# Kernel tuning notes

Measured on AMD Instinct MI355X. Metric: run time of the kernel, lower is better.

## Reference

```python
import jax, jax.numpy as jnp
import numpy as np

N_NODES = 50000
N_EDGES = 640000
HID = 128
EDGE_FEAT = 4
NUM_G = 20
R_MIN, R_MAX = 0.0, 10.0

def setup_inputs() -> dict:
    key = jax.random.key(0)
    ks = jax.random.split(key, 16)
    s = lambda d: 1.0 / np.sqrt(d)
    return {
        'h': jax.random.normal(ks[0], (N_NODES, HID), jnp.float32),
        'x': jax.random.normal(ks[1], (N_NODES, 3), jnp.float32),
        'edge_index': jax.random.randint(ks[2], (2, N_EDGES), 0, N_NODES, dtype=jnp.int64),
        'mask_ligand': jnp.ones((N_NODES,), jnp.float32),
        'edge_attr': jax.random.normal(ks[3], (N_EDGES, EDGE_FEAT), jnp.float32),
        'We1': jax.random.normal(ks[4], (2*HID+EDGE_FEAT+NUM_G, HID), jnp.float32) * s(2*HID+EDGE_FEAT+NUM_G),
        'be1': jnp.zeros((HID,), jnp.float32),
        'We2': jax.random.normal(ks[5], (HID, HID), jnp.float32) * s(HID),
        'be2': jnp.zeros((HID,), jnp.float32),
        'Winf': jax.random.normal(ks[6], (HID, 1), jnp.float32) * s(HID),
        'binf': jnp.zeros((1,), jnp.float32),
        'Wx1': jax.random.normal(ks[7], (HID, HID), jnp.float32) * s(HID),
        'bx1': jnp.zeros((HID,), jnp.float32),
        'Wx2': jax.random.normal(ks[8], (HID, 1), jnp.float32) * 0.001 * s(HID),
        'Wn1': jax.random.normal(ks[9], (2*HID, HID), jnp.float32) * s(2*HID),
        'bn1': jnp.zeros((HID,), jnp.float32),
        'Wn2': jax.random.normal(ks[10], (HID, HID), jnp.float32) * s(HID),
        'bn2': jnp.zeros((HID,), jnp.float32),
    }

def reference(h, x, edge_index, mask_ligand, edge_attr,
              We1, be1, We2, be2, Winf, binf, Wx1, bx1, Wx2, Wn1, bn1, Wn2, bn2):
    n = h.shape[0]
    src, dst = edge_index[0], edge_index[1]
    hi, hj = h[dst], h[src]                      # [E, H] gathers
    rel_x = x[dst] - x[src]                      # [E, 3]
    d_sq = jnp.sum(rel_x**2, axis=-1, keepdims=True)  # [E, 1]
    d = jnp.sqrt(d_sq + 1e-8)
    # GaussianSmearing(r_min=0, r_max=10, num_gaussians=20)
    offset = jnp.linspace(R_MIN, R_MAX, NUM_G, dtype=h.dtype)
    coeff = -0.5 / (offset[1] - offset[0])**2
    d_feat = jnp.exp(coeff * (d - offset)**2)    # [E, 20]
    edge_feat = jnp.concatenate([d_feat, edge_attr], axis=-1)
    # edge MLP (2 layers, silu, act_last=True)
    z = jnp.concatenate([hi, hj, edge_feat], axis=-1)
    mij = jax.nn.silu(jax.nn.silu(z @ We1 + be1) @ We2 + be2)  # [E, H]
    eij = jax.nn.sigmoid(mij @ Winf + binf)      # [E, 1]
    mi = jax.ops.segment_sum(mij * eij, dst, num_segments=n)   # [N, H]
    # node MLP (2 layers, silu, no act on last)
    nz = jnp.concatenate([mi, h], axis=-1)
    h_out = h + (jax.nn.silu(nz @ Wn1 + bn1) @ Wn2 + bn2)
    # coordinate update
    xg = jnp.tanh(jax.nn.silu(mij @ Wx1 + bx1) @ Wx2)          # [E, 1]
    delta_x = jax.ops.segment_sum(rel_x / (d + 1.0) * xg, dst, num_segments=n)
    x_out = x + delta_x * mask_ligand[:, None]
    return h_out, x_out
```

## Files before the change

### kernel.cpp

```cpp
#include <hip/hip_runtime.h>
#include <math.h>

#define NN 50000
#define NE 640000
#define H 128
#define EPB 64
#define NPB 64
#define ZB 280
#define BB 136
#define KP1 288
#define NZB 264
#define NBPAD 50176
#define HISTB (NE / 256)
#define CONVB 464
#define ALLOCB (NBPAD / 256)
#define HCONVB 3125
#define N4OUT ((NN * H + NN * 3) / 4)
#define ZOB ((N4OUT + 255) / 256)

typedef __attribute__((ext_vector_type(8))) unsigned short u16x8;
typedef __attribute__((ext_vector_type(8))) __bf16 bf16x8;
typedef __attribute__((ext_vector_type(2))) __bf16 bf16x2;
typedef __attribute__((ext_vector_type(4))) float f32x4;

__device__ __forceinline__ float frcp(float x) {
#if __has_builtin(__builtin_amdgcn_rcpf)
    return __builtin_amdgcn_rcpf(x);
#else
    return 1.0f / x;
#endif
}

__device__ __forceinline__ float silu_f(float v) {
    return v * frcp(1.0f + __expf(-v));
}

__device__ __forceinline__ float sigmoid_f(float v) {
    return frcp(1.0f + __expf(-v));
}

__device__ __forceinline__ float tanh_f(float v) {
    return 1.0f - 2.0f * frcp(1.0f + __expf(2.0f * v));
}

__device__ __forceinline__ unsigned short f2bf(float f) {
    unsigned int u = __builtin_bit_cast(unsigned int, f);
    u += 0x7FFFu + ((u >> 16) & 1u);
    return (unsigned short)(u >> 16);
}

__device__ __forceinline__ float bf2f(unsigned short s) {
    unsigned int u = ((unsigned int)s) << 16;
    return __builtin_bit_cast(float, u);
}

__device__ __forceinline__ unsigned int pkbf(float lo, float hi) {
#if __has_builtin(__builtin_amdgcn_cvt_pk_bf16_f32)
    bf16x2 v = __builtin_amdgcn_cvt_pk_bf16_f32(lo, hi);
    unsigned int r; __builtin_memcpy(&r, &v, 4); return r;
#else
    return (unsigned int)f2bf(lo) | ((unsigned int)f2bf(hi) << 16);
#endif
}

__device__ __forceinline__ f32x4 mfma16(u16x8 a, u16x8 b, f32x4 c) {
    return __builtin_amdgcn_mfma_f32_16x16x32_bf16(
        __builtin_bit_cast(bf16x8, a), __builtin_bit_cast(bf16x8, b), c, 0, 0, 0);
}

__global__ __launch_bounds__(256) void init_small_kernel(
    float4* __restrict__ p, int n4)
{
    int i = blockIdx.x * 256 + threadIdx.x;
    if (i < n4) p[i] = make_float4(0.f, 0.f, 0.f, 0.f);
}

__global__ __launch_bounds__(256) void hist_conv_zero_kernel(
    const int* __restrict__ ei, int* __restrict__ cnt, int histBlocks,
    const float* __restrict__ We1, const float* __restrict__ We2,
    const float* __restrict__ Wx1, const float* __restrict__ Wn1,
    const float* __restrict__ Wn2,
    unsigned short* __restrict__ w1t, unsigned short* __restrict__ w2t,
    unsigned short* __restrict__ wx1t, unsigned short* __restrict__ wn1t,
    unsigned short* __restrict__ wn2t,
    float4* __restrict__ out4)
{
    int b = blockIdx.x, t = threadIdx.x;
    if (b < histBlocks) {
        atomicAdd(&cnt[ei[NE + b * 256 + t]], 1);
        return;
    }
    b -= histBlocks;
    if (b < CONVB) {
        int i = b * 256 + t;
        const int S1 = 128 * KP1;
        const int S2 = 128 * 128;
        const int S3 = 128 * 256;
        if (i < S1) {
            int n = i / KP1, k = i % KP1;
            w1t[i] = (k < 280) ? f2bf(We1[k * H + n]) : (unsigned short)0;
        } else if (i < S1 + S2) {
            int j = i - S1; int n = j / H, k = j % H;
            w2t[j] = f2bf(We2[k * H + n]);
        } else if (i < S1 + 2 * S2) {
            int j = i - S1 - S2; int n = j / H, k = j % H;
            wx1t[j] = f2bf(Wx1[k * H + n]);
        } else if (i < S1 + 2 * S2 + S3) {
            int j = i - S1 - 2 * S2; int n = j / 256, k = j % 256;
            wn1t[j] = f2bf(Wn1[k * H + n]);
        } else if (i < S1 + 3 * S2 + S3) {
            int j = i - S1 - 2 * S2 - S3; int n = j / H, k = j % H;
            wn2t[j] = f2bf(Wn2[k * H + n]);
        }
        return;
    }
    b -= CONVB;
    int i = b * 256 + t;
    if (i < N4OUT) out4[i] = make_float4(0.f, 0.f, 0.f, 0.f);
}

__global__ __launch_bounds__(256) void alloc_kernel(
    const int* __restrict__ cnt, int* __restrict__ cur, int* __restrict__ gtot)
{
    int t = threadIdx.x;
    int d = blockIdx.x * 256 + t;
    int v = cnt[d];
    int incl = v;
    #pragma unroll
    for (int o = 1; o < 64; o <<= 1) {
        int u = __shfl_up(incl, o, 64);
        if ((t & 63) >= o) incl += u;
    }
    int total = __shfl(incl, 63, 64);
    int base = 0;
    if ((t & 63) == 63) base = atomicAdd(gtot, total);
    base = __shfl(base, 63, 64);
    cur[d] = base + incl - v;
}

__global__ __launch_bounds__(256) void scatter_hconv_kernel(
    const int* __restrict__ ei, const float* __restrict__ edge_attr,
    int* __restrict__ cur, uint4* __restrict__ epay,
    const float* __restrict__ h, unsigned short* __restrict__ hb)
{
    int b = blockIdx.x, t = threadIdx.x;
    if (b < NE / 256) {
        int i = b * 256 + t;
        int s = ei[i], d = ei[NE + i];
        float4 ea = ((const float4*)edge_attr)[i];
        int p = atomicAdd(&cur[d], 1);
        uint4 pv = { (unsigned)s, (unsigned)d, pkbf(ea.x, ea.y), pkbf(ea.z, ea.w) };
        epay[p] = pv;
        return;
    }
    int j = (b - NE / 256) * 256 + t;
    const float4* hp = (const float4*)h + (size_t)j * 2;
    float4 a = hp[0], c = hp[1];
    uint4 pk = { pkbf(a.x, a.y), pkbf(a.z, a.w), pkbf(c.x, c.y), pkbf(c.z, c.w) };
    ((uint4*)hb)[j] = pk;
}

__global__ __launch_bounds__(512, 6) void edge_kernel(
    const float* __restrict__ h, const float* __restrict__ x,
    const int* __restrict__ ei, const float* __restrict__ edge_attr,
    const unsigned short* __restrict__ w1t, const float* __restrict__ be1,
    const unsigned short* __restrict__ w2t, const float* __restrict__ be2,
    const float* __restrict__ Winf, const float* __restrict__ binf,
    const unsigned short* __restrict__ wx1t, const float* __restrict__ bx1,
    const float* __restrict__ Wx2,
    const uint4* __restrict__ epay, const unsigned short* __restrict__ hb,
    float* __restrict__ mi, float* __restrict__ dx)
{
    __shared__ unsigned short zs[EPB * ZB + 8];
    __shared__ float relx_s[EPB][3];
    __shared__ float eij_acc[EPB];
    __shared__ float xg_acc[EPB];
    __shared__ int dst_s[EPB];
    __shared__ float winf_s[H];
    __shared__ float wx2_s[H];

    unsigned short* m1 = zs;
    unsigned short* m2 = zs + EPB * BB;

    const int t = threadIdx.x;
    int bid = blockIdx.x;
    if ((gridDim.x & 7) == 0) {
        int cpx = gridDim.x >> 3;
        bid = (bid & 7) * cpx + (bid >> 3);
    }
    const int e0 = bid * EPB;
    const bool srt = (epay != nullptr);

    if (t >= 128 && t < 256) {
        winf_s[t - 128] = Winf[t - 128];
        wx2_s[t - 128] = Wx2[t - 128];
    } else if (t >= 256 && t < 320) {
        eij_acc[t - 256] = binf[0];
        xg_acc[t - 256] = 0.f;
    } else if (t == 320) {
        uint4 zf = {0u, 0u, 0u, 0u};
        *(uint4*)(zs + EPB * ZB) = zf;
    }

    {
        int e = t >> 3, l = t & 7;
        unsigned short* zr = zs + e * ZB;
        if (srt) {
            uint4 pv = epay[e0 + e];
            const uint4* hd = (const uint4*)(hb + (size_t)pv.y * H);
            const uint4* hs = (const uint4*)(hb + (size_t)pv.x * H);
            uint4 a0 = hd[l * 2], a1 = hd[l * 2 + 1];
            *(uint4*)(zr + l * 16) = a0;
            *(uint4*)(zr + l * 16 + 8) = a1;
            uint4 c0 = hs[l * 2], c1 = hs[l * 2 + 1];
            *(uint4*)(zr + 128 + l * 16) = c0;
            *(uint4*)(zr + 128 + l * 16 + 8) = c1;
        } else {
            int s = ei[e0 + e], d = ei[NE + e0 + e];
            const float4* hd = (const float4*)(h + (size_t)d * H);
            const float4* hs = (const float4*)(h + (size_t)s * H);
            float4 v0 = hd[l * 4 + 0], v1 = hd[l * 4 + 1];
            float4 v2 = hd[l * 4 + 2], v3 = hd[l * 4 + 3];
            uint4 p0 = { pkbf(v0.x, v0.y), pkbf(v0.z, v0.w), pkbf(v1.x, v1.y), pkbf(v1.z, v1.w) };
            uint4 p1 = { pkbf(v2.x, v2.y), pkbf(v2.z, v2.w), pkbf(v3.x, v3.y), pkbf(v3.z, v3.w) };
            *(uint4*)(zr + l * 16) = p0;
            *(uint4*)(zr + l * 16 + 8) = p1;
            float4 w0 = hs[l * 4 + 0], w1 = hs[l * 4 + 1];
            float4 w2 = hs[l * 4 + 2], w3 = hs[l * 4 + 3];
            uint4 q0 = { pkbf(w0.x, w0.y), pkbf(w0.z, w0.w), pkbf(w1.x, w1.y), pkbf(w1.z, w1.w) };
            uint4 q1 = { pkbf(w2.x, w2.y), pkbf(w2.z, w2.w), pkbf(w3.x, w3.y), pkbf(w3.z, w3.w) };
            *(uint4*)(zr + 128 + l * 16) = q0;
            *(uint4*)(zr + 128 + l * 16 + 8) = q1;
        }
    }
    if (t < EPB) {
        unsigned short* zr = zs + t * ZB;
        int s, d;
        if (srt) {
            uint4 pv = epay[e0 + t];
            s = (int)pv.x; d = (int)pv.y;
            *(unsigned int*)(zr + 276) = pv.z;
            *(unsigned int*)(zr + 278) = pv.w;
        } else {
            s = ei[e0 + t]; d = ei[NE + e0 + t];
            #pragma unroll
            for (int j = 0; j < 4; j++)
                zr[276 + j] = f2bf(edge_attr[(size_t)(e0 + t) * 4 + j]);
        }
        dst_s[t] = d;
        float rx = x[d * 3 + 0] - x[s * 3 + 0];
        float ry = x[d * 3 + 1] - x[s * 3 + 1];
        float rz = x[d * 3 + 2] - x[s * 3 + 2];
        float d2 = rx * rx + ry * ry + rz * rz;
        float dd = sqrtf(d2 + 1e-8f);
        float inv = frcp(dd + 1.0f);
        relx_s[t][0] = rx * inv;
        relx_s[t][1] = ry * inv;
        relx_s[t][2] = rz * inv;
        const float step = 10.0f / 19.0f;
        const float coeff = -0.5f / (step * step);
        #pragma unroll
        for (int g = 0; g < 20; g++) {
            float df = dd - step * (float)g;
            zr[256 + g] = f2bf(__expf(coeff * df * df));
        }
    }
    __syncthreads();

    const int wv = t >> 6, lane = t & 63;
    const int quad = lane >> 4, r16 = lane & 15;
    const int F = wv * 16;
    const int f0 = F + quad * 4;

    {
        f32x4 acc[4] = {};
        #pragma unroll
        for (int ks = 0; ks < KP1 / 32; ks++) {
            int ko = ks * 32 + quad * 8;
            u16x8 a = *(const u16x8*)(w1t + (size_t)(F + r16) * KP1 + ko);
            #pragma unroll
            for (int ci = 0; ci < 4; ci++) {
                u16x8 b = *(const u16x8*)(zs + (ci * 16 + r16) * ZB + ko);
                acc[ci] = mfma16(a, b, acc[ci]);
            }
        }
        __syncthreads();
        float4 bv = *(const float4*)(be1 + f0);
        #pragma unroll
        for (int ci = 0; ci < 4; ci++) {
            int e = ci * 16 + r16;
            float s0 = silu_f(acc[ci][0] + bv.x);
            float s1 = silu_f(acc[ci][1] + bv.y);
            float s2 = silu_f(acc[ci][2] + bv.z);
            float s3 = silu_f(acc[ci][3] + bv.w);
            uint2 p = { pkbf(s0, s1), pkbf(s2, s3) };
            *(uint2*)(m1 + e * BB + f0) = p;
        }
    }
    __syncthreads();

    {
        f32x4 acc[4] = {};
        #pragma unroll
        for (int ks = 0; ks < H / 32; ks++) {
            int ko = ks * 32 + quad * 8;
            u16x8 a = *(const u16x8*)(w2t + (size_t)(F + r16) * H + ko);
            #pragma unroll
            for (int ci = 0; ci < 4; ci++) {
                u16x8 b = *(const u16x8*)(m1 + (ci * 16 + r16) * BB + ko);
                acc[ci] = mfma16(a, b, acc[ci]);
            }
        }
        float4 bv = *(const float4*)(be2 + f0);
        float4 wf = *(const float4*)(winf_s + f0);
        float ep[4];
        #pragma unroll
        for (int ci = 0; ci < 4; ci++) {
            int e = ci * 16 + r16;
            float s0 = silu_f(acc[ci][0] + bv.x);
            float s1 = silu_f(acc[ci][1] + bv.y);
            float s2 = silu_f(acc[ci][2] + bv.z);
            float s3 = silu_f(acc[ci][3] + bv.w);
            ep[ci] = s0 * wf.x + s1 * wf.y + s2 * wf.z + s3 * wf.w;
            uint2 p = { pkbf(s0, s1), pkbf(s2, s3) };
            *(uint2*)(m2 + e * BB + f0) = p;
        }
        #pragma unroll
        for (int ci = 0; ci < 4; ci++) {
            ep[ci] += __shfl_xor(ep[ci], 16, 64);
            ep[ci] += __shfl_xor(ep[ci], 32, 64);
        }
        if (quad == 0) {
            #pragma unroll
            for (int ci = 0; ci < 4; ci++)
                atomicAdd(&eij_acc[ci * 16 + r16], ep[ci]);
        }
    }
    __syncthreads();

    if (t < EPB) eij_acc[t] = sigmoid_f(eij_acc[t]);

    {
        f32x4 acc[4] = {};
        #pragma unroll
        for (int ks = 0; ks < H / 32; ks++) {
            int ko = ks * 32 + quad * 8;
            u16x8 a = *(const u16x8*)(wx1t + (size_t)(F + r16) * H + ko);
            #pragma unroll
            for (int ci = 0; ci < 4; ci++) {
                u16x8 b = *(const u16x8*)(m2 + (ci * 16 + r16) * BB + ko);
                acc[ci] = mfma16(a, b, acc[ci]);
            }
        }
        float4 bv = *(const float4*)(bx1 + f0);
        float4 wf = *(const float4*)(wx2_s + f0);
        float xp[4];
        #pragma unroll
        for (int ci = 0; ci < 4; ci++) {
            xp[ci] = silu_f(acc[ci][0] + bv.x) * wf.x
                   + silu_f(acc[ci][1] + bv.y) * wf.y
                   + silu_f(acc[ci][2] + bv.z) * wf.z
                   + silu_f(acc[ci][3] + bv.w) * wf.w;
        }
        #pragma unroll
        for (int ci = 0; ci < 4; ci++) {
            xp[ci] += __shfl_xor(xp[ci], 16, 64);
            xp[ci] += __shfl_xor(xp[ci], 32, 64);
        }
        if (quad == 0) {
            #pragma unroll
            for (int ci = 0; ci < 4; ci++)
                atomicAdd(&xg_acc[ci * 16 + r16], xp[ci]);
        }
    }
    __syncthreads();

    if (t < 128) {
        const int k = t;
        float acc = 0.f;
        int rs = 0;
        #pragma unroll
        for (int c = 0; c < EPB; c += 8) {
            float v[8];
            #pragma unroll
            for (int j = 0; j < 8; j++)
                v[j] = bf2f(m2[(c + j) * BB + k]) * eij_acc[c + j];
            #pragma unroll
            for (int j = 0; j < 8; j++) {
                int e = c + j;
                acc += v[j];
                if (e == EPB - 1 || dst_s[e + 1] != dst_s[e]) {
                    float* p = &mi[(size_t)dst_s[e] * H + k];
                    if (srt && rs > 0 && e < EPB - 1) *p = acc;
                    else atomicAdd(p, acc);
                    acc = 0.f;
                    rs = e + 1;
                }
            }
        }
    } else if (t < 131) {
        const int dd = t - 128;
        float acc = 0.f;
        int rs = 0;
        #pragma unroll
        for (int c = 0; c < EPB; c += 8) {
            float v[8];
            #pragma unroll
            for (int j = 0; j < 8; j++)
                v[j] = relx_s[c + j][dd] * tanh_f(xg_acc[c + j]);
            #pragma unroll
            for (int j = 0; j < 8; j++) {
                int e = c + j;
                acc += v[j];
                if (e == EPB - 1 || dst_s[e + 1] != dst_s[e]) {
                    float* p = &dx[(size_t)dst_s[e] * 3 + dd];
                    if (srt && rs > 0 && e < EPB - 1) *p = acc;
                    else atomicAdd(p, acc);
                    acc = 0.f;
                    rs = e + 1;
                }
            }
        }
    }
}

__global__ __launch_bounds__(512, 6) void node_kernel(
    const float* __restrict__ h, const float* __restrict__ x,
    const float* __restrict__ mask,
    const unsigned short* __restrict__ wn1t, const float* __restrict__ bn1,
    const unsigned short* __restrict__ wn2t, const float* __restrict__ bn2,
    const unsigned short* __restrict__ hb,
    float* __restrict__ mi_hout, float* __restrict__ dx_xout)
{
    __shared__ unsigned short nzs[NPB * NZB];

    unsigned short* nbuf = nzs;

    const int t = threadIdx.x;
    const int n0 = blockIdx.x * NPB;

    {
        int r = t >> 3, l = t & 7;
        int n = n0 + r;
        unsigned short* zr = nzs + r * NZB;
        if (n < NN) {
            const float4* mi4 = (const float4*)(mi_hout + (size_t)n * H);
            float4 v0 = mi4[l * 4 + 0], v1 = mi4[l * 4 + 1];
            float4 v2 = mi4[l * 4 + 2], v3 = mi4[l * 4 + 3];
            uint4 p0 = { pkbf(v0.x, v0.y), pkbf(v0.z, v0.w), pkbf(v1.x, v1.y), pkbf(v1.z, v1.w) };
            uint4 p1 = { pkbf(v2.x, v2.y), pkbf(v2.z, v2.w), pkbf(v3.x, v3.y), pkbf(v3.z, v3.w) };
            *(uint4*)(zr + l * 16) = p0;
            *(uint4*)(zr + l * 16 + 8) = p1;
            if (hb) {
                const uint4* hs = (const uint4*)(hb + (size_t)n * H);
                *(uint4*)(zr + 128 + l * 16) = hs[l * 2];
                *(uint4*)(zr + 128 + l * 16 + 8) = hs[l * 2 + 1];
            } else {
                const float4* h4 = (const float4*)(h + (size_t)n * H);
                float4 w0 = h4[l * 4 + 0], w1 = h4[l * 4 + 1];
                float4 w2 = h4[l * 4 + 2], w3 = h4[l * 4 + 3];
                uint4 q0 = { pkbf(w0.x, w0.y), pkbf(w0.z, w0.w), pkbf(w1.x, w1.y), pkbf(w1.z, w1.w) };
                uint4 q1 = { pkbf(w2.x, w2.y), pkbf(w2.z, w2.w), pkbf(w3.x, w3.y), pkbf(w3.z, w3.w) };
                *(uint4*)(zr + 128 + l * 16) = q0;
                *(uint4*)(zr + 128 + l * 16 + 8) = q1;
            }
        } else {
            uint4 zf = {0u, 0u, 0u, 0u};
            *(uint4*)(zr + l * 16) = zf;
            *(uint4*)(zr + l * 16 + 8) = zf;
            *(uint4*)(zr + 128 + l * 16) = zf;
            *(uint4*)(zr + 128 + l * 16 + 8) = zf;
        }
    }

    float xo = 0.f;
    int xn = -1, xdim = 0;
    if (t < NPB * 3) {
        int r = t / 3; xdim = t % 3;
        int n = n0 + r;
        if (n < NN) {
            xn = n;
            xo = x[(size_t)n * 3 + xdim] + dx_xout[(size_t)n * 3 + xdim] * mask[n];
        }
    }
    __syncthreads();

    if (xn >= 0) dx_xout[(size_t)xn * 3 + xdim] = xo;

    const int wv = t >> 6, lane = t & 63;
    const int quad = lane >> 4, r16 = lane & 15;
    const int F = wv * 16;
    const int f0 = F + quad * 4;

    {
        f32x4 acc[4] = {};
        #pragma unroll
        for (int ks = 0; ks < 2 * H / 32; ks++) {
            int ko = ks * 32 + quad * 8;
            u16x8 a = *(const u16x8*)(wn1t + (size_t)(F + r16) * (2 * H) + ko);
            #pragma unroll
            for (int ci = 0; ci < 4; ci++) {
                u16x8 b = *(const u16x8*)(nzs + (ci * 16 + r16) * NZB + ko);
                acc[ci] = mfma16(a, b, acc[ci]);
            }
        }
        __syncthreads();
        float4 bv = *(const float4*)(bn1 + f0);
        #pragma unroll
        for (int ci = 0; ci < 4; ci++) {
            int e = ci * 16 + r16;
            float s0 = silu_f(acc[ci][0] + bv.x);
            float s1 = silu_f(acc[ci][1] + bv.y);
            float s2 = silu_f(acc[ci][2] + bv.z);
            float s3 = silu_f(acc[ci][3] + bv.w);
            uint2 p = { pkbf(s0, s1), pkbf(s2, s3) };
            *(uint2*)(nbuf + e * BB + f0) = p;
        }
    }
    __syncthreads();

    {
        f32x4 acc[4] = {};
        #pragma unroll
        for (int ks = 0; ks < H / 32; ks++) {
            int ko = ks * 32 + quad * 8;
            u16x8 a = *(const u16x8*)(wn2t + (size_t)(F + r16) * H + ko);
            #pragma unroll
            for (int ci = 0; ci < 4; ci++) {
                u16x8 b = *(const u16x8*)(nbuf + (ci * 16 + r16) * BB + ko);
                acc[ci] = mfma16(a, b, acc[ci]);
            }
        }
        float4 bv = *(const float4*)(bn2 + f0);
        #pragma unroll
        for (int ci = 0; ci < 4; ci++) {
            int n = n0 + ci * 16 + r16;
            if (n < NN) {
                float4 hv = *(const float4*)(h + (size_t)n * H + f0);
                float4 o;
                o.x = hv.x + acc[ci][0] + bv.x;
                o.y = hv.y + acc[ci][1] + bv.y;
                o.z = hv.z + acc[ci][2] + bv.z;
                o.w = hv.w + acc[ci][3] + bv.w;
                *(float4*)(mi_hout + (size_t)n * H + f0) = o;
            }
        }
    }
}

extern "C" void kernel_launch(void* const* d_in, const int* in_sizes, int n_in,
                              void* d_out, int out_size, void* d_ws, size_t ws_size,
                              hipStream_t stream) {
    const float* h     = (const float*)d_in[0];
    const float* x     = (const float*)d_in[1];
    const int*   ei    = (const int*)d_in[2];
    const float* mask  = (const float*)d_in[3];
    const float* eattr = (const float*)d_in[4];
    const float* We1   = (const float*)d_in[5];
    const float* be1   = (const float*)d_in[6];
    const float* We2   = (const float*)d_in[7];
    const float* be2   = (const float*)d_in[8];
    const float* Winf  = (const float*)d_in[9];
    const float* binf  = (const float*)d_in[10];
    const float* Wx1   = (const float*)d_in[11];
    const float* bx1   = (const float*)d_in[12];
    const float* Wx2   = (const float*)d_in[13];
    const float* Wn1   = (const float*)d_in[14];
    const float* bn1   = (const float*)d_in[15];
    const float* Wn2   = (const float*)d_in[16];
    const float* bn2   = (const float*)d_in[17];

    float* mi = (float*)d_out;
    float* dx = mi + (size_t)NN * H;

    char* wsb  = (char*)d_ws;
    unsigned short* w1t  = (unsigned short*)wsb;
    unsigned short* w2t  = w1t + 128 * KP1;
    unsigned short* wx1t = w2t + 128 * H;
    unsigned short* wn1t = wx1t + 128 * H;
    unsigned short* wn2t = wn1t + 128 * 256;

    const size_t OFF_CNT  = 262144;
    const size_t OFF_GTOT = OFF_CNT + (size_t)NBPAD * 4;
    const size_t OFF_CUR  = OFF_GTOT + 16;
    const size_t OFF_HB   = OFF_CUR + (size_t)NBPAD * 4;
    const size_t OFF_EPAY = OFF_HB + (size_t)NN * H * 2;
    const size_t WS_NEED  = OFF_EPAY + (size_t)NE * 16;

    int*   cnt  = (int*)(wsb + OFF_CNT);
    int*   gtot = (int*)(wsb + OFF_GTOT);
    int*   cur  = (int*)(wsb + OFF_CUR);
    unsigned short* hb = (unsigned short*)(wsb + OFF_HB);
    uint4* epay = (uint4*)(wsb + OFF_EPAY);

    const bool full = (ws_size >= WS_NEED);

    if (full) {
        const int n4c = (int)((OFF_CUR - OFF_CNT) / 16);
        init_small_kernel<<<(n4c + 255) / 256, 256, 0, stream>>>(
            (float4*)(wsb + OFF_CNT), n4c);
    }

    {
        int hb_ = full ? HISTB : 0;
        hist_conv_zero_kernel<<<hb_ + CONVB + ZOB, 256, 0, stream>>>(
            ei, cnt, hb_, We1, We2, Wx1, Wn1, Wn2,
            w1t, w2t, wx1t, wn1t, wn2t, (float4*)d_out);
    }

    if (full) {
        alloc_kernel<<<ALLOCB, 256, 0, stream>>>(cnt, cur, gtot);
        scatter_hconv_kernel<<<NE / 256 + HCONVB, 256, 0, stream>>>(
            ei, eattr, cur, epay, h, hb);
    }

    edge_kernel<<<NE / EPB, 512, 0, stream>>>(
        h, x, ei, eattr, w1t, be1, w2t, be2, Winf, binf, wx1t, bx1, Wx2,
        full ? epay : (const uint4*)nullptr,
        full ? hb : (const unsigned short*)nullptr,
        mi, dx);

    node_kernel<<<(NN + NPB - 1) / NPB, 512, 0, stream>>>(
        h, x, mask, wn1t, bn1, wn2t, bn2,
        full ? hb : (const unsigned short*)nullptr,
        mi, dx);
}
```

Before: 443.8 us.

## Replace LDS atomics with per-wave partial sums and move h conversion earlier

The edge kernel's per-edge eij and xg reductions now write per-wave partials into shared arrays, which are summed by 64 threads after a barrier. This replaces shared-memory atomicAdd and hoists the tanh so it is computed once per edge. The zs row stride grows from 280 to 296 with in-row zero padding, replacing the single trailing pad, which may change bank-conflict behaviour. The h-to-bf16 conversion moves from the scatter kernel into the earlier histogram/convert kernel, leaving scatter as edges only. The cost is one extra barrier and more LDS per block.

```diff
diff --git a/kernel.cpp b/kernel.cpp
--- a/kernel.cpp
+++ b/kernel.cpp
@@ -6,7 +6,7 @@
 #define H 128
 #define EPB 64
 #define NPB 64
-#define ZB 280
+#define ZB 296
 #define BB 136
 #define KP1 288
 #define NZB 264
@@ -75,7 +75,7 @@
     if (i < n4) p[i] = make_float4(0.f, 0.f, 0.f, 0.f);
 }
 
-__global__ __launch_bounds__(256) void hist_conv_zero_kernel(
+__global__ __launch_bounds__(256) void hist_conv_zero_hconv_kernel(
     const int* __restrict__ ei, int* __restrict__ cnt, int histBlocks,
     const float* __restrict__ We1, const float* __restrict__ We2,
     const float* __restrict__ Wx1, const float* __restrict__ Wn1,
@@ -83,7 +83,8 @@
     unsigned short* __restrict__ w1t, unsigned short* __restrict__ w2t,
     unsigned short* __restrict__ wx1t, unsigned short* __restrict__ wn1t,
     unsigned short* __restrict__ wn2t,
-    float4* __restrict__ out4)
+    float4* __restrict__ out4,
+    const float* __restrict__ h, unsigned short* __restrict__ hb)
 {
     int b = blockIdx.x, t = threadIdx.x;
     if (b < histBlocks) {
@@ -115,8 +116,17 @@
         return;
     }
     b -= CONVB;
-    int i = b * 256 + t;
-    if (i < N4OUT) out4[i] = make_float4(0.f, 0.f, 0.f, 0.f);
+    if (b < ZOB) {
+        int i = b * 256 + t;
+        if (i < N4OUT) out4[i] = make_float4(0.f, 0.f, 0.f, 0.f);
+        return;
+    }
+    b -= ZOB;
+    int j = b * 256 + t;
+    const float4* hp = (const float4*)h + (size_t)j * 2;
+    float4 a = hp[0], c = hp[1];
+    uint4 pk = { pkbf(a.x, a.y), pkbf(a.z, a.w), pkbf(c.x, c.y), pkbf(c.z, c.w) };
+    ((uint4*)hb)[j] = pk;
 }
 
 __global__ __launch_bounds__(256) void alloc_kernel(
@@ -138,26 +148,16 @@
     cur[d] = base + incl - v;
 }
 
-__global__ __launch_bounds__(256) void scatter_hconv_kernel(
+__global__ __launch_bounds__(256) void scatter_kernel(
     const int* __restrict__ ei, const float* __restrict__ edge_attr,
-    int* __restrict__ cur, uint4* __restrict__ epay,
-    const float* __restrict__ h, unsigned short* __restrict__ hb)
+    int* __restrict__ cur, uint4* __restrict__ epay)
 {
-    int b = blockIdx.x, t = threadIdx.x;
-    if (b < NE / 256) {
-        int i = b * 256 + t;
-        int s = ei[i], d = ei[NE + i];
-        float4 ea = ((const float4*)edge_attr)[i];
-        int p = atomicAdd(&cur[d], 1);
-        uint4 pv = { (unsigned)s, (unsigned)d, pkbf(ea.x, ea.y), pkbf(ea.z, ea.w) };
-        epay[p] = pv;
-        return;
-    }
-    int j = (b - NE / 256) * 256 + t;
-    const float4* hp = (const float4*)h + (size_t)j * 2;
-    float4 a = hp[0], c = hp[1];
-    uint4 pk = { pkbf(a.x, a.y), pkbf(a.z, a.w), pkbf(c.x, c.y), pkbf(c.z, c.w) };
-    ((uint4*)hb)[j] = pk;
+    int i = blockIdx.x * 256 + threadIdx.x;
+    int s = ei[i], d = ei[NE + i];
+    float4 ea = ((const float4*)edge_attr)[i];
+    int p = atomicAdd(&cur[d], 1);
+    uint4 pv = { (unsigned)s, (unsigned)d, pkbf(ea.x, ea.y), pkbf(ea.z, ea.w) };
+    epay[p] = pv;
 }
 
 __global__ __launch_bounds__(512, 6) void edge_kernel(
@@ -171,10 +171,12 @@
     const uint4* __restrict__ epay, const unsigned short* __restrict__ hb,
     float* __restrict__ mi, float* __restrict__ dx)
 {
-    __shared__ unsigned short zs[EPB * ZB + 8];
+    __shared__ unsigned short zs[EPB * ZB];
     __shared__ float relx_s[EPB][3];
-    __shared__ float eij_acc[EPB];
-    __shared__ float xg_acc[EPB];
+    __shared__ float eij_s[EPB];
+    __shared__ float xg_s[EPB];
+    __shared__ float epart[8][EPB];
+    __shared__ float xpart[8][EPB];
     __shared__ int dst_s[EPB];
     __shared__ float winf_s[H];
     __shared__ float wx2_s[H];
@@ -194,12 +196,6 @@
     if (t >= 128 && t < 256) {
         winf_s[t - 128] = Winf[t - 128];
         wx2_s[t - 128] = Wx2[t - 128];
-    } else if (t >= 256 && t < 320) {
-        eij_acc[t - 256] = binf[0];
-        xg_acc[t - 256] = 0.f;
-    } else if (t == 320) {
-        uint4 zf = {0u, 0u, 0u, 0u};
-        *(uint4*)(zs + EPB * ZB) = zf;
     }
 
     {
@@ -264,6 +260,8 @@
             float df = dd - step * (float)g;
             zr[256 + g] = f2bf(__expf(coeff * df * df));
         }
+        #pragma unroll
+        for (int j = 280; j < ZB; j++) zr[j] = 0;
     }
     __syncthreads();
 
@@ -333,12 +331,17 @@
         if (quad == 0) {
             #pragma unroll
             for (int ci = 0; ci < 4; ci++)
-                atomicAdd(&eij_acc[ci * 16 + r16], ep[ci]);
+                epart[wv][ci * 16 + r16] = ep[ci];
         }
     }
     __syncthreads();
 
-    if (t < EPB) eij_acc[t] = sigmoid_f(eij_acc[t]);
+    if (t < EPB) {
+        float s = binf[0];
+        #pragma unroll
+        for (int w = 0; w < 8; w++) s += epart[w][t];
+        eij_s[t] = sigmoid_f(s);
+    }
 
     {
         f32x4 acc[4] = {};
@@ -370,8 +373,16 @@
         if (quad == 0) {
             #pragma unroll
             for (int ci = 0; ci < 4; ci++)
-                atomicAdd(&xg_acc[ci * 16 + r16], xp[ci]);
-        }
+                xpart[wv][ci * 16 + r16] = xp[ci];
+        }
+    }
+    __syncthreads();
+
+    if (t < EPB) {
+        float xs = 0.f;
+        #pragma unroll
+        for (int w = 0; w < 8; w++) xs += xpart[w][t];
+        xg_s[t] = tanh_f(xs);
     }
     __syncthreads();
 
@@ -384,7 +395,7 @@
             float v[8];
             #pragma unroll
             for (int j = 0; j < 8; j++)
-                v[j] = bf2f(m2[(c + j) * BB + k]) * eij_acc[c + j];
+                v[j] = bf2f(m2[(c + j) * BB + k]) * eij_s[c + j];
             #pragma unroll
             for (int j = 0; j < 8; j++) {
                 int e = c + j;
@@ -407,7 +418,7 @@
             float v[8];
             #pragma unroll
             for (int j = 0; j < 8; j++)
-                v[j] = relx_s[c + j][dd] * tanh_f(xg_acc[c + j]);
+                v[j] = relx_s[c + j][dd] * xg_s[c + j];
             #pragma unroll
             for (int j = 0; j < 8; j++) {
                 int e = c + j;
@@ -603,15 +614,15 @@
 
     {
         int hb_ = full ? HISTB : 0;
-        hist_conv_zero_kernel<<<hb_ + CONVB + ZOB, 256, 0, stream>>>(
+        int hc_ = full ? HCONVB : 0;
+        hist_conv_zero_hconv_kernel<<<hb_ + CONVB + ZOB + hc_, 256, 0, stream>>>(
             ei, cnt, hb_, We1, We2, Wx1, Wn1, Wn2,
-            w1t, w2t, wx1t, wn1t, wn2t, (float4*)d_out);
+            w1t, w2t, wx1t, wn1t, wn2t, (float4*)d_out, h, hb);
     }
 
     if (full) {
         alloc_kernel<<<ALLOCB, 256, 0, stream>>>(cnt, cur, gtot);
-        scatter_hconv_kernel<<<NE / 256 + HCONVB, 256, 0, stream>>>(
-            ei, eattr, cur, epay, h, hb);
+        scatter_kernel<<<NE / 256, 256, 0, stream>>>(ei, eattr, cur, epay);
     }
 
     edge_kernel<<<NE / EPB, 512, 0, stream>>>(
```

After: 425.9 us. 1.04x faster.
